# Optimization experiments

Measured on AMD Instinct MI355X. Metric: run time of the kernel, lower is better.

The kernel has to match this reference:

```python
import jax, jax.numpy as jnp
import numpy as np

# Eval-mode reference (dropout disabled), faithful to run_specGCN_lstm(reconstruct_graph=True).

def _run_lstm(x, h0, c0, wih, whh, b):
    # x: [B, T, in]; wih: [4H, in]; torch gate order i, f, g, o
    def step(carry, xt):
        h, c = carry
        g = xt @ wih.T + h @ whh.T + b
        i, f, gg, o = jnp.split(g, 4, axis=-1)
        c = jax.nn.sigmoid(f) * c + jax.nn.sigmoid(i) * jnp.tanh(gg)
        h = jax.nn.sigmoid(o) * jnp.tanh(c)
        return (h, c), h
    (h, c), ys = jax.lax.scan(step, (h0, c0), jnp.swapaxes(x, 0, 1))
    return jnp.swapaxes(ys, 0, 1), h, c


def _lstm2(x, states, wih0, whh0, b0, wih1, whh1, b1):
    (h0, c0), (h1, c1) = states
    y0, hf0, cf0 = _run_lstm(x, h0, c0, wih0, whh0, b0)
    y1, hf1, cf1 = _run_lstm(y0, h1, c1, wih1, whh1, b1)
    return y1, ((hf0, cf0), (hf1, cf1))


def setup_inputs() -> dict:
    key = jax.random.key(0)
    ks = jax.random.split(key, 20)
    B, D, Y, N, F, O, H = 256, 28, 7, 23, 128, 64, 128
    s_gl = 1.0 / np.sqrt(F)
    s_gcn = np.sqrt(6.0 / (F + O)) * 1.414
    s_l0 = 1.0 / np.sqrt(H)
    return {
        "x": jax.random.normal(ks[0], (B, D, N, F), jnp.float32),
        "adj_real": jax.random.uniform(ks[1], (B, D, N, N), jnp.float32),
        "infection": jax.random.uniform(ks[2], (B, D, N), jnp.float32),
        "day_order": jax.random.randint(ks[3], (B,), 0, 10, jnp.int32),
        "gl_w1": jax.random.normal(ks[4], (F, F), jnp.float32) * s_gl,
        "gl_b1": jax.random.normal(ks[5], (F,), jnp.float32) * s_gl,
        "gl_w2": jax.random.normal(ks[6], (F, F), jnp.float32) * s_gl,
        "gl_b2": jax.random.normal(ks[7], (F,), jnp.float32) * s_gl,
        "glp": jax.random.normal(ks[8], (N, N), jnp.float32) * 0.1,
        "gcn_w": jax.random.uniform(ks[9], (F, O), jnp.float32, -s_gcn, s_gcn),
        "v": jnp.full((N,), 0.05, jnp.float32),  # torch init: mean 0.05, std 0
        "lstm_wih0": jax.random.normal(ks[10], (4 * H, O + 1), jnp.float32) * s_l0,
        "lstm_whh0": jax.random.normal(ks[11], (4 * H, H), jnp.float32) * s_l0,
        "lstm_b0": jax.random.normal(ks[12], (4 * H,), jnp.float32) * s_l0,
        "lstm_wih1": jax.random.normal(ks[13], (4 * H, H), jnp.float32) * s_l0,
        "lstm_whh1": jax.random.normal(ks[14], (4 * H, H), jnp.float32) * s_l0,
        "lstm_b1": jax.random.normal(ks[15], (4 * H,), jnp.float32) * s_l0,
        "fc_w": jax.random.normal(ks[16], (1, H + D), jnp.float32) * 0.05,
        "fc_b": jax.random.normal(ks[17], (1,), jnp.float32) * 0.05,
    }


def reference(x, adj_real, infection, day_order, gl_w1, gl_b1, gl_w2, gl_b2,
              glp, gcn_w, v, lstm_wih0, lstm_whh0, lstm_b0, lstm_wih1,
              lstm_whh1, lstm_b1, fc_w, fc_b):
    B, D, N, F = x.shape
    O = gcn_w.shape[1]
    H = lstm_whh0.shape[1]
    Y = 7  # y_days
    alpha = 1.0

    # GraphLearner (alpha = 1)
    n1 = jnp.tanh(alpha * (x @ gl_w1.T + gl_b1))  # [B,D,N,F]
    n2 = jnp.tanh(alpha * (x @ gl_w2.T + gl_b2))
    s12 = jnp.einsum('bdnf,bdmf->bdnm', n1, n2)
    adj_learned = jax.nn.relu(jnp.tanh(alpha * (s12 - jnp.swapaxes(s12, -1, -2))))

    # degree-gated real adjacency
    deg = adj_real.sum(-1)  # [B,D,N]
    mat_deg = jax.nn.sigmoid(glp * (deg[..., :, None] * deg[..., None, :]))
    adj = adj_learned + mat_deg * adj_real  # adj_output [B,D,N,N]

    # SpecGCN: D^-1/2 (A+I) D^-1/2, then X W, relu (dropout off in eval)
    tA = adj + jnp.eye(N, dtype=adj.dtype)
    dinv = tA.sum(-1) ** -0.5
    dad = dinv[..., :, None] * tA * dinv[..., None, :]
    gcn = jax.nn.relu(jnp.einsum('bdnm,bdmo->bdno', dad, x @ gcn_w))  # [B,D,N,O]

    # per-zone temporal decay exp(v^2 * day_order)
    factor = jnp.exp(v * v * day_order.astype(x.dtype)[:, None])  # [B,N]
    gcn = gcn * factor[:, None, :, None]

    lstm_in = jnp.concatenate([gcn, infection[..., None]], axis=-1)  # [B,D,N,O+1]
    zin = jnp.transpose(lstm_in, (2, 0, 1, 3)).reshape(N * B, D, O + 1)

    z0 = jnp.zeros((N * B, H), x.dtype)
    zeros = ((z0, z0), (z0, z0))
    _, states = _lstm2(zin, zeros, lstm_wih0, lstm_whh0, lstm_b0,
                       lstm_wih1, lstm_whh1, lstm_b1)

    x2 = jnp.broadcast_to(zin.mean(axis=1, keepdims=True), (N * B, Y, O + 1))
    out, _ = _lstm2(x2, states, lstm_wih0, lstm_whh0, lstm_b0,
                    lstm_wih1, lstm_whh1, lstm_b1)  # [NB, Y, H]

    inf_feat = jnp.transpose(infection, (2, 0, 1)).reshape(N * B, 1, D)
    inf_feat = jnp.broadcast_to(inf_feat, (N * B, Y, D))
    fc_in = jnp.concatenate([out, inf_feat], axis=-1)  # [NB, Y, H+D]
    y = jax.nn.relu(fc_in @ fc_w.T + fc_b)  # [NB, Y, 1]
    y_out = jnp.transpose(y.reshape(N, B, Y), (1, 2, 0))  # [B, Y, N]
    return adj, y_out
```

## Files before the change

kernel.cpp:

```cpp
#include <hip/hip_runtime.h>
#include <hip/hip_bf16.h>
#include <stdint.h>


#define DB 256
#define DD 28
#define DN 23
#define DF 128
#define DO 64
#define DH 128
#define DY 7
#define NBSEQ (DN*DB)
#define ADJSZ (DB*DD*DN*DN)
#define GBLK 184
#define L2E 1.4426950408889634f

#define WB0_OFF   47480832u
#define WB1_OFF   47710208u
#define WPK_OFF   47972352u
#define GPK_OFF   48103424u

using v8bf  = __attribute__((ext_vector_type(8))) __bf16;
using f32x4 = __attribute__((ext_vector_type(4))) float;
using u32x4 = __attribute__((ext_vector_type(4))) unsigned int;
using u16x4 = __attribute__((ext_vector_type(4))) unsigned short;

__device__ __forceinline__ float fsig(float x)  { return 1.f/(1.f+__expf(-x)); }
__device__ __forceinline__ float ftanh(float x) { return 1.f - 2.f/(__expf(2.f*x)+1.f); }
__device__ __forceinline__ float fsigR(float x){
    return __builtin_amdgcn_rcpf(1.f + __builtin_amdgcn_exp2f(-x*L2E));
}
__device__ __forceinline__ float ftanhR(float x){
    return 1.f - 2.f*__builtin_amdgcn_rcpf(__builtin_amdgcn_exp2f(x*(2.f*L2E))+1.f);
}
__device__ __forceinline__ float fsig2(float a){
    return __builtin_amdgcn_rcpf(1.f + __builtin_amdgcn_exp2f(-a));
}
__device__ __forceinline__ float ftanh2(float a){
    return 1.f - 2.f*__builtin_amdgcn_rcpf(__builtin_amdgcn_exp2f(a)+1.f);
}
__device__ __forceinline__ float ftanhc(float c){
    return 1.f - 2.f*__builtin_amdgcn_rcpf(__builtin_amdgcn_exp2f(c*(2.f*L2E))+1.f);
}

__device__ __forceinline__ unsigned short f2bf(float f){
    unsigned u = __builtin_bit_cast(unsigned, f);
    return (unsigned short)((u + 0x7FFFu + ((u>>16)&1u)) >> 16);
}
__device__ __forceinline__ float bf2f(unsigned short b){
    return __builtin_bit_cast(float, (unsigned)b << 16);
}
__device__ __forceinline__ uint4 ntload4(const uint4* p){
    u32x4 v = __builtin_nontemporal_load((const u32x4*)p);
    return *(uint4*)&v;
}
__device__ __forceinline__ unsigned pkbf(float lo, float hi){
    unsigned r;
    asm("v_cvt_pk_bf16_f32 %0, %1, %2" : "=v"(r) : "v"(lo), "v"(hi));
    return r;
}

#define MFMA_(acc_, A_, B_) acc_ = __builtin_amdgcn_mfma_f32_16x16x32_bf16(A_, B_, acc_, 0, 0, 0)

__global__ __launch_bounds__(256) void kernPrep(
    const float* __restrict__ wih0, const float* __restrict__ whh0,
    const float* __restrict__ wih1, const float* __restrict__ whh1,
    const float* __restrict__ glw1, const float* __restrict__ glw2,
    const float* __restrict__ gcn_w,
    unsigned short* __restrict__ wb0, unsigned short* __restrict__ wb1,
    unsigned short* __restrict__ wpk, unsigned short* __restrict__ gpk)
{
    int idx = blockIdx.x*256 + threadIdx.x;
    if (idx < 114688){
        int e = idx&7, l = (idx>>3)&63, mt = (idx>>9)&31, kt = idx>>14;
        int rit = l&15, lj = rit>>2, g = rit&3;
        int r = g*128 + (mt>>2)*16 + lj*4 + (mt&3);
        int k = kt*32 + (l>>4)*8 + e;
        float v = 0.f;
        if (k < 65)                  v = wih0[r*65 + k];
        else if (k >= 72 && k < 200) v = whh0[r*128 + (k-72)];
        v *= (g==2) ? (2.f*L2E) : L2E;
        wb0[idx] = f2bf(v);
        return;
    }
    idx -= 114688;
    if (idx < 131072){
        int e = idx&7, l = (idx>>3)&63, mt = (idx>>9)&31, kt = idx>>14;
        int rit = l&15, lj = rit>>2, g = rit&3;
        int r = g*128 + (mt>>2)*16 + lj*4 + (mt&3);
        int k = kt*32 + (l>>4)*8 + e;
        float v = (k < 128) ? wih1[r*128 + k] : whh1[r*128 + (k-128)];
        v *= (g==2) ? (2.f*L2E) : L2E;
        wb1[idx] = f2bf(v);
        return;
    }
    idx -= 131072;
    if (idx < 65536){
        int e = idx&7, l = (idx>>3)&63, hsel = (idx>>9)&1, kt = (idx>>10)&3,
            nt = (idx>>12)&7, mat = (idx>>15)&1;
        int fo = nt*16 + (l&15);
        int k  = kt*32 + (l>>4)*8 + e;
        float v = (mat ? glw2 : glw1)[fo*128 + k];
        unsigned short hb = f2bf(v);
        wpk[idx] = hsel ? f2bf(v - bf2f(hb)) : hb;
        return;
    }
    idx -= 65536;
    if (idx < 8192){
        int e = idx&7, l = (idx>>3)&63, kt = (idx>>9)&3, nt = (idx>>11)&3;
        int o = nt*16 + (l&15);
        int k = kt*32 + (l>>4)*8 + e;
        gpk[idx] = f2bf(gcn_w[k*64 + o]);
    }
}

__global__ __launch_bounds__(256) void kernA(
    const float* __restrict__ x, const float* __restrict__ adj_real,
    const float* __restrict__ infection, const int* __restrict__ day_order,
    const float* __restrict__ b1, const float* __restrict__ b2,
    const float* __restrict__ glp, const float* __restrict__ vvec,
    const v8bf* __restrict__ wpk, const v8bf* __restrict__ gpk,
    float* __restrict__ out_adj, uint4* __restrict__ zlin4)
{
    const int bd = blockIdx.x;
    const int b  = bd / DD;
    const int t  = threadIdx.x;
    const int w  = t>>6, l = t&63;

    __shared__ float sm[4140];
    const int S12=0, ADJ=552, XW=1104, DEG=2576, DINV=2599, FACT=2622,
              INFS=2645, GC=2668;
    __shared__ __align__(16) unsigned short xhl[2][32][140];
    __shared__ __align__(16) unsigned short n1b[32*136];
    __shared__ __align__(16) unsigned short n2b[32*136];
    unsigned short* n1l = &xhl[0][0][0];
    unsigned short* n2l = n1l + 32*136;

    {
        const float4* xg4 = (const float4*)(x + (size_t)bd*(DN*DF));
        for (int p=t; p<736; p+=256){
            float4 v = xg4[p];
            int n = p>>5, k4 = (p&31)<<2;
            unsigned short h0=f2bf(v.x), h1=f2bf(v.y), h2=f2bf(v.z), h3=f2bf(v.w);
            u16x4 hv = {h0,h1,h2,h3};
            u16x4 lv = {f2bf(v.x-bf2f(h0)), f2bf(v.y-bf2f(h1)),
                        f2bf(v.z-bf2f(h2)), f2bf(v.w-bf2f(h3))};
            *(u16x4*)&xhl[0][n][k4] = hv;
            *(u16x4*)&xhl[1][n][k4] = lv;
        }
    }
    for (int p=t; p<9*DF; p+=256){
        int n = DN + (p>>7), k = p&127;
        xhl[0][n][k] = 0; xhl[1][n][k] = 0;
    }
    {
        const float* arg = adj_real + (size_t)bd*(DN*DN);
        for (int p=t; p<DN*DN; p+=256){
            int i = p/DN, j = p - i*DN;
            sm[ADJ + i*24 + j] = arg[p];
        }
    }
    {
        uint4 z; z.x=z.y=z.z=z.w=0u;
        for (int i=t; i<306; i+=256){
            int bsel = (i >= 153), off = bsel ? i-153 : i;
            *(uint4*)((char*)(bsel ? n2b : n1b) + 6256 + off*16) = z;
        }
    }
    if (t < DN){
        float vv = vvec[t];
        sm[FACT+t] = __expf(vv*vv*(float)day_order[b]);
        sm[INFS+t] = infection[(size_t)bd*DN + t];
    }
    __syncthreads();

    {
        f32x4 acc2[2];
        { f32x4 z; z[0]=z[1]=z[2]=z[3]=0.f; acc2[0]=z; acc2[1]=z; }
        #pragma unroll
        for (int kt=0;kt<4;kt++){
            v8bf ah[2], al[2];
            #pragma unroll
            for (int mt=0;mt<2;mt++){
                int m = mt*16 + (l&15);
                int ko = (l>>4)*8 + kt*32;
                ah[mt] = *(const v8bf*)&xhl[0][m][ko];
                al[mt] = *(const v8bf*)&xhl[1][m][ko];
            }
            v8bf gh = gpk[(size_t)(w*4+kt)*64 + l];
            MFMA_(acc2[0], ah[0], gh);
            MFMA_(acc2[1], ah[1], gh);
            MFMA_(acc2[0], al[0], gh);
            MFMA_(acc2[1], al[1], gh);
        }
        int o = w*16 + (l&15);
        #pragma unroll
        for (int mt=0;mt<2;mt++){
            #pragma unroll
            for (int r=0;r<4;r++){
                int n = mt*16 + (l>>4)*4 + r;
                if (n < DN) sm[XW + n*64 + o] = acc2[mt][r];
            }
        }
    }

    if (t < DN){
        float s = 0.f;
        for (int m=0;m<DN;m++) s += sm[ADJ + t*24 + m];
        sm[DEG+t] = s;
    }

    {
        const int mat = w>>1;
        const int ntb = (w&1)*4;
        const float* bsrc = mat ? b2 : b1;
        float bias[4];
        #pragma unroll
        for (int q=0;q<4;q++) bias[q] = bsrc[(ntb+q)*16 + (l&15)];
        f32x4 acc[2][4];
        #pragma unroll
        for (int mt=0;mt<2;mt++)
            #pragma unroll
            for (int q=0;q<4;q++){ f32x4 z; z[0]=z[1]=z[2]=z[3]=0.f; acc[mt][q]=z; }
        #pragma unroll
        for (int kt=0;kt<4;kt++){
            v8bf ah[2], al[2];
            #pragma unroll
            for (int mt=0;mt<2;mt++){
                int m = mt*16 + (l&15);
                int ko = (l>>4)*8 + kt*32;
                ah[mt] = *(const v8bf*)&xhl[0][m][ko];
                al[mt] = *(const v8bf*)&xhl[1][m][ko];
            }
            #pragma unroll
            for (int q=0;q<4;q++){
                const v8bf* wb = wpk + ((size_t)(((mat*8+(ntb+q))*4+kt)*2)*64 + l);
                v8bf wh = wb[0], wl = wb[64];
                MFMA_(acc[0][q], ah[0], wh);
                MFMA_(acc[1][q], ah[1], wh);
                MFMA_(acc[0][q], al[0], wh);
                MFMA_(acc[1][q], al[1], wh);
                MFMA_(acc[0][q], ah[0], wl);
                MFMA_(acc[1][q], ah[1], wl);
            }
        }
        __syncthreads();

        unsigned short* dsth = mat ? n2b : n1b;
        unsigned short* dstl = mat ? n2l : n1l;
        #pragma unroll
        for (int mt=0;mt<2;mt++){
            #pragma unroll
            for (int q=0;q<4;q++){
                int fo = (ntb+q)*16 + (l&15);
                #pragma unroll
                for (int r=0;r<4;r++){
                    int n = mt*16 + (l>>4)*4 + r;
                    if (n < DN){
                        float nv = ftanhR(acc[mt][q][r] + bias[q]);
                        unsigned short hb = f2bf(nv);
                        dsth[n*136 + fo] = hb;
                        dstl[n*136 + fo] = f2bf(nv - bf2f(hb));
                    }
                }
            }
        }
        {
            uint4 z; z.x=z.y=z.z=z.w=0u;
            for (int i=t; i<306; i+=256){
                int bsel = (i >= 153), off = bsel ? i-153 : i;
                *(uint4*)((char*)(bsel ? n2l : n1l) + 6256 + off*16) = z;
            }
        }
    }
    __syncthreads();

    {
        const int mt = w>>1, nt = w&1;
        f32x4 a3; a3[0]=a3[1]=a3[2]=a3[3]=0.f;
        #pragma unroll
        for (int kt=0;kt<4;kt++){
            int ar = (mt*16+(l&15))*136 + kt*32 + (l>>4)*8;
            int br = (nt*16+(l&15))*136 + kt*32 + (l>>4)*8;
            v8bf ah  = *(const v8bf*)&n1b[ar];
            v8bf alo = *(const v8bf*)&n1l[ar];
            v8bf bh  = *(const v8bf*)&n2b[br];
            v8bf blo = *(const v8bf*)&n2l[br];
            MFMA_(a3, ah,  bh);
            MFMA_(a3, alo, bh);
            MFMA_(a3, ah,  blo);
        }
        #pragma unroll
        for (int r=0;r<4;r++){
            int i = mt*16 + (l>>4)*4 + r;
            int j = nt*16 + (l&15);
            if (i < DN && j < DN) sm[S12 + i*24 + j] = a3[r];
        }
    }
    __syncthreads();

    for (int p=t; p<DN*DN; p+=256){
        int i=p/DN, j=p-i*DN;
        float al  = fmaxf(ftanhR(sm[S12+i*24+j]-sm[S12+j*24+i]), 0.f);
        float md  = fsigR(glp[i*DN+j]*sm[DEG+i]*sm[DEG+j]);
        float arv = sm[ADJ + i*24 + j];
        float adjv = al + md*arv;
        __builtin_nontemporal_store(adjv, &out_adj[(size_t)bd*(DN*DN) + p]);
        sm[ADJ + i*24 + j] = adjv + (i==j ? 1.f : 0.f);
    }
    __syncthreads();

    if (t<DN){
        float rs=0.f;
        for (int jj=0;jj<DN;jj++) rs += sm[ADJ+t*24+jj];
        sm[DINV+t] = rsqrtf(rs);
    }
    __syncthreads();

    for (int p=t;p<DN*DN;p+=256){
        int i=p/DN, j=p-i*DN;
        sm[ADJ+i*24+j] *= sm[DINV+i]*sm[DINV+j];
    }
    __syncthreads();

    for (int p=t;p<DN*64;p+=256){
        int n=p>>6, o=p&63;
        float a=0.f;
        #pragma unroll
        for (int m=0;m<DN;m++) a = fmaf(sm[ADJ+n*24+m], sm[XW+m*64+o], a);
        sm[GC + p] = fmaxf(a,0.f)*sm[FACT+n];
    }
    __syncthreads();

    for (int p=t; p<DN*18; p+=256){
        int n = p/18, r = p - n*18, hsel = r/9, k8 = r - hsel*9;
        __align__(16) unsigned short ob[8];
        #pragma unroll
        for (int e=0;e<8;e++){
            int k = k8*8+e;
            float v = (k<64) ? sm[GC + n*64 + k] : ((k==64) ? sm[INFS+n] : 0.f);
            unsigned short hb = f2bf(v);
            ob[e] = hsel ? f2bf(v - bf2f(hb)) : hb;
        }
        zlin4[(size_t)bd*414 + p] = *(const uint4*)ob;
    }
}

#define XB0O 0
#define XB1O 4608
#define U1H0 9216
#define U1H1 28672
#define X2O  45056
#define B0O  54272
#define B1O  56320
#define FCO  58368
#define INO  58896
#define C0O  59024
#define C1O  75408

__global__ __launch_bounds__(1024, 2) void kernB(
    const uint4* __restrict__ zlin, const v8bf* __restrict__ w0p, const v8bf* __restrict__ w1p,
    const float* __restrict__ b0g, const float* __restrict__ b1g,
    const float* __restrict__ infection, const float* __restrict__ fcw,
    const float* __restrict__ fcb, float* __restrict__ outy)
{
    const int t = threadIdx.x, blk = blockIdx.x;
    const int w = t>>6, l = t&63;
    const int lhi = l>>4, llo = l&15;
    __shared__ __align__(16) unsigned char smraw[91792];
    char* smb = (char*)smraw;

    {
        uint4 z; z.x=z.y=z.z=z.w=0u;
        for (int i = t; i < (54272-9216)/16; i += 1024) ((uint4*)(smb+9216))[i] = z;
        for (int i = t; i < (91792-59024)/16; i += 1024) ((uint4*)(smb+59024))[i] = z;
    }
    if (t < 512){
        float s = ((t&3)==2) ? (2.f*L2E) : L2E;
        ((float*)(smb+B0O))[t] = b0g[(t&3)*128 + (t>>2)] * s;
        ((float*)(smb+B1O))[t] = b1g[(t&3)*128 + (t>>2)] * s;
    }
    if (t < 129) ((float*)(smb+FCO))[t] = (t<128) ? fcw[t] : fcb[0];
    if (t < 32){
        int gseq = blk*32 + t, n = gseq>>8, bb = gseq&255;
        float a = 0.f;
        for (int dd=0; dd<DD; dd++)
            a = fmaf(fcw[128+dd], infection[((size_t)bb*DD+dd)*DN+n], a);
        ((float*)(smb+INO))[t] = a;
    }

    int k81 = t >> 5, sq1 = t & 31;
    int gs1 = blk*32 + sq1;
    size_t cb1 = (size_t)(gs1 & 255)*DD*414 + (gs1>>8)*18 + k81;
    int d1 = t*16;

    const int mt0 = 2*w;
    const int jt  = mt0>>2, r3 = mt0&3;
    const int j8  = jt*2 + (lhi>>1);
    const int sub = (lhi&1)*8 + r3*2;
    const int j0  = jt*16 + lhi*4 + r3;

    __syncthreads();

    if (t < 288){
        uint4 a0 = ntload4(zlin + cb1);
        *(uint4*)(smb + XB0O + d1) = a0;
    }
    __syncthreads();

    for (int step = 0; step < DD + DY; ++step){
        const int ps  = step & 1;
        const int xb  = ps ? XB1O : XB0O;
        const int xbn = ps ? XB0O : XB1O;
        const bool do_stage = (step + 1 < DD);
        const char* h0rd = smb + U1H0 + (ps^1)*9728;
        char*       h0wr = smb + U1H0 + ps*9728;
        const char* h1rd = smb + U1H1 + (ps^1)*8192;
        char*       h1wr = smb + U1H1 + ps*8192;

        {
            uint4 sv0; sv0.x=sv0.y=sv0.z=sv0.w=0u;
            if (do_stage && t < 288)
                sv0 = ntload4(zlin + (size_t)(step+1)*414 + cb1);

            f32x4 acc[2][2];
            #pragma unroll
            for (int mi=0;mi<2;mi++){
                f32x4 bv = *(const f32x4*)(smb + B0O + (j0+mi)*16);
                acc[mi][0] = bv; acc[mi][1] = bv;
            }
            #pragma unroll 2
            for (int kt=0; kt<7; ++kt){
                const v8bf* wrow = w0p + (size_t)(kt*32 + mt0)*64 + l;
                v8bf A0 = wrow[0], A1 = wrow[64];
                int k8 = kt*4 + lhi;
                bool inx = (k8 <= 8);
                const char* hib = inx ? (smb + xb + k8*512) : (h0rd + (k8-9)*512);
                v8bf BH0 = *(const v8bf*)(hib + llo*16);
                v8bf BH1 = *(const v8bf*)(hib + 256 + llo*16);
                MFMA_(acc[0][0], A0, BH0);
                MFMA_(acc[1][0], A1, BH0);
                MFMA_(acc[0][1], A0, BH1);
                MFMA_(acc[1][1], A1, BH1);
            }
            if (do_stage && t < 288)
                *(uint4*)(smb + xbn + d1) = sv0;

            if (step < DD && t < 288){
                const unsigned short* hp = (const unsigned short*)(smb + xb + t*16);
                float* xs = (float*)(smb + X2O);
                #pragma unroll
                for (int e=0;e<8;e++) xs[e*288+t] += bf2f(hp[e]);
            }

            {
                f32x4 c0v = *(const f32x4*)(smb + C0O + t*16);
                #pragma unroll
                for (int nt=0;nt<2;nt++){
                    float hf[2];
                    #pragma unroll
                    for (int mi=0;mi<2;mi++){
                        f32x4 a = acc[mi][nt];
                        float ii = fsig2(a[0]), ff = fsig2(a[1]), gg = ftanh2(a[2]), oo = fsig2(a[3]);
                        float c = ff*c0v[mi*2+nt] + ii*gg;
                        c0v[mi*2+nt] = c;
                        hf[mi] = oo*ftanhc(c);
                    }
                    unsigned ph = pkbf(hf[0], hf[1]);
                    int bo = j8*512 + (nt*16+llo)*16 + sub;
                    *(unsigned*)(h0wr + bo) = ph;
                }
                *(f32x4*)(smb + C0O + t*16) = c0v;
            }
            __syncthreads();
        }

        {
            f32x4 acc1[2][2];
            #pragma unroll
            for (int mi=0;mi<2;mi++){
                f32x4 bv = *(const f32x4*)(smb + B1O + (j0+mi)*16);
                acc1[mi][0] = bv; acc1[mi][1] = bv;
            }
            #pragma unroll 2
            for (int kt=0; kt<8; ++kt){
                const v8bf* wrow = w1p + (size_t)(kt*32 + mt0)*64 + l;
                v8bf A0 = wrow[0], A1 = wrow[64];
                int k8 = kt*4 + lhi;
                const char* hib = (k8 < 16) ? (h0wr + k8*512) : (h1rd + (k8-16)*512);
                v8bf BH0 = *(const v8bf*)(hib + llo*16);
                v8bf BH1 = *(const v8bf*)(hib + 256 + llo*16);
                MFMA_(acc1[0][0], A0, BH0);
                MFMA_(acc1[1][0], A1, BH0);
                MFMA_(acc1[0][1], A0, BH1);
                MFMA_(acc1[1][1], A1, BH1);
            }

            {
                f32x4 c1v = *(const f32x4*)(smb + C1O + t*16);
                #pragma unroll
                for (int nt=0;nt<2;nt++){
                    float hf[2];
                    #pragma unroll
                    for (int mi=0;mi<2;mi++){
                        f32x4 a = acc1[mi][nt];
                        float ii = fsig2(a[0]), ff = fsig2(a[1]), gg = ftanh2(a[2]), oo = fsig2(a[3]);
                        float c = ff*c1v[mi*2+nt] + ii*gg;
                        c1v[mi*2+nt] = c;
                        hf[mi] = oo*ftanhc(c);
                    }
                    unsigned ph = pkbf(hf[0], hf[1]);
                    int bo = j8*512 + (nt*16+llo)*16 + sub;
                    *(unsigned*)(h1wr + bo) = ph;
                }
                *(f32x4*)(smb + C1O + t*16) = c1v;
            }
        }

        if (step == DD-1){
            __syncthreads();
            if (t < 288){
                const float* xs = (const float*)(smb + X2O);
                __align__(16) unsigned short hb8[8];
                #pragma unroll
                for (int e=0;e<8;e++) hb8[e] = f2bf(xs[e*288+t] * (1.f/(float)DD));
                *(uint4*)(smb + XB0O + t*16) = *(const uint4*)hb8;
                *(uint4*)(smb + XB1O + t*16) = *(const uint4*)hb8;
            }
            __syncthreads();
        }

        if (step >= DD){
            __syncthreads();
            if (t < 256){
                int seq = t>>3, l8 = t&7;
                const unsigned short* uh = (const unsigned short*)(smb + U1H1 + ps*8192);
                const float* fw = (const float*)(smb+FCO);
                float a = 0.f;
                #pragma unroll
                for (int half=0; half<2; ++half){
                    int k8 = l8*2 + half;
                    int base = (k8*32 + seq)*8;
                    #pragma unroll
                    for (int e=0;e<8;e++){
                        int j = l8*16 + half*8 + e;
                        a = fmaf(fw[j], bf2f(uh[base+e]), a);
                    }
                }
                a += __shfl_down(a, 4, 8);
                a += __shfl_down(a, 2, 8);
                a += __shfl_down(a, 1, 8);
                if (l8 == 0){
                    int gseq = blk*32 + seq, n = gseq>>8, bb = gseq&255;
                    float yv = fmaxf(a + ((const float*)(smb+INO))[seq] + fw[128], 0.f);
                    __builtin_nontemporal_store(yv, &outy[((size_t)bb*DY + (step-DD))*DN + n]);
                }
            }
        }
    }
}

extern "C" void kernel_launch(void* const* d_in, const int* in_sizes, int n_in,
                              void* d_out, int out_size, void* d_ws, size_t ws_size,
                              hipStream_t stream)
{
    const float* x         = (const float*)d_in[0];
    const float* adj_real  = (const float*)d_in[1];
    const float* infection = (const float*)d_in[2];
    const int*   day_order = (const int*)  d_in[3];
    const float* gl_w1     = (const float*)d_in[4];
    const float* gl_b1     = (const float*)d_in[5];
    const float* gl_w2     = (const float*)d_in[6];
    const float* gl_b2     = (const float*)d_in[7];
    const float* glp       = (const float*)d_in[8];
    const float* gcn_w     = (const float*)d_in[9];
    const float* vvec      = (const float*)d_in[10];
    const float* wih0      = (const float*)d_in[11];
    const float* whh0      = (const float*)d_in[12];
    const float* b0        = (const float*)d_in[13];
    const float* wih1      = (const float*)d_in[14];
    const float* whh1      = (const float*)d_in[15];
    const float* b1        = (const float*)d_in[16];
    const float* fcw       = (const float*)d_in[17];
    const float* fcb       = (const float*)d_in[18];

    uint8_t* wsb = (uint8_t*)d_ws;
    uint4*          zlin = (uint4*)(wsb);
    unsigned short* wb0  = (unsigned short*)(wsb + WB0_OFF);
    unsigned short* wb1  = (unsigned short*)(wsb + WB1_OFF);
    unsigned short* wpk  = (unsigned short*)(wsb + WPK_OFF);
    unsigned short* gpk  = (unsigned short*)(wsb + GPK_OFF);
    float* out_adj = (float*)d_out;
    float* out_y   = out_adj + ADJSZ;

    kernPrep<<<dim3(1248), dim3(256), 0, stream>>>(wih0, whh0, wih1, whh1,
                                                   gl_w1, gl_w2, gcn_w,
                                                   wb0, wb1, wpk, gpk);
    kernA<<<dim3(DB*DD), dim3(256), 0, stream>>>(x, adj_real, infection, day_order,
                                                 gl_b1, gl_b2, glp, vvec,
                                                 (const v8bf*)wpk, (const v8bf*)gpk,
                                                 out_adj, zlin);
    kernB<<<dim3(GBLK), dim3(1024), 0, stream>>>(zlin, (const v8bf*)wb0,
                                                 (const v8bf*)wb1, b0, b1, infection,
                                                 fcw, fcb, out_y);
}
```

Before: 297.2 us.

## Precompute sequence mean in separate kernel and prefetch first layer-1 weight tile

Moves the time-mean of the LSTM input out of the recurrent kernel into a new small kernel, kernM, that reads zlin and writes a bf16 mean buffer. The recurrent kernel then stages the mean as its input for the prediction steps, which removes the per-step shared-memory accumulation and the two extra barriers at the step boundary. It also loads the first k-tile of the layer-1 weights early so that load overlaps the layer-0 gate math, and it shrinks shared memory. The cost is an extra kernel launch and a re-read of zlin, and the mean is now summed from bf16 hi/lo halves separately, which changes rounding slightly.

```diff
diff --git a/kernel.cpp b/kernel.cpp
--- a/kernel.cpp
+++ b/kernel.cpp
@@ -19,6 +19,7 @@
 #define WB1_OFF   47710208u
 #define WPK_OFF   47972352u
 #define GPK_OFF   48103424u
+#define ZME_OFF   48119808u
 
 using v8bf  = __attribute__((ext_vector_type(8))) __bf16;
 using f32x4 = __attribute__((ext_vector_type(4))) float;
@@ -114,6 +115,30 @@
     }
 }
 
+__global__ __launch_bounds__(256) void kernM(
+    const uint4* __restrict__ zlin, uint4* __restrict__ zmean)
+{
+    int idx = blockIdx.x*256 + threadIdx.x;
+    if (idx >= GBLK*288) return;
+    int blk = idx/288, u = idx - blk*288;
+    int k8 = u>>5, sq = u&31;
+    int gs = blk*32 + sq, bb = gs&255, nn = gs>>8;
+    const uint4* src = zlin + (size_t)bb*DD*414 + nn*18 + k8;
+    float s[8];
+    #pragma unroll
+    for (int e=0;e<8;e++) s[e]=0.f;
+    for (int d=0; d<DD; ++d){
+        uint4 v = src[(size_t)d*414];
+        const unsigned short* hp = (const unsigned short*)&v;
+        #pragma unroll
+        for (int e=0;e<8;e++) s[e] += bf2f(hp[e]);
+    }
+    __align__(16) unsigned short ob[8];
+    #pragma unroll
+    for (int e=0;e<8;e++) ob[e] = f2bf(s[e]*(1.f/(float)DD));
+    zmean[idx] = *(const uint4*)ob;
+}
+
 __global__ __launch_bounds__(256) void kernA(
     const float* __restrict__ x, const float* __restrict__ adj_real,
     const float* __restrict__ infection, const int* __restrict__ day_order,
@@ -350,16 +375,16 @@
 #define XB1O 4608
 #define U1H0 9216
 #define U1H1 28672
-#define X2O  45056
-#define B0O  54272
-#define B1O  56320
-#define FCO  58368
-#define INO  58896
-#define C0O  59024
-#define C1O  75408
+#define B0O  45056
+#define B1O  47104
+#define FCO  49152
+#define INO  49680
+#define C0O  49808
+#define C1O  66192
 
 __global__ __launch_bounds__(1024, 2) void kernB(
-    const uint4* __restrict__ zlin, const v8bf* __restrict__ w0p, const v8bf* __restrict__ w1p,
+    const uint4* __restrict__ zlin, const uint4* __restrict__ zmean,
+    const v8bf* __restrict__ w0p, const v8bf* __restrict__ w1p,
     const float* __restrict__ b0g, const float* __restrict__ b1g,
     const float* __restrict__ infection, const float* __restrict__ fcw,
     const float* __restrict__ fcb, float* __restrict__ outy)
@@ -367,13 +392,13 @@
     const int t = threadIdx.x, blk = blockIdx.x;
     const int w = t>>6, l = t&63;
     const int lhi = l>>4, llo = l&15;
-    __shared__ __align__(16) unsigned char smraw[91792];
+    __shared__ __align__(16) unsigned char smraw[82576];
     char* smb = (char*)smraw;
 
     {
         uint4 z; z.x=z.y=z.z=z.w=0u;
-        for (int i = t; i < (54272-9216)/16; i += 1024) ((uint4*)(smb+9216))[i] = z;
-        for (int i = t; i < (91792-59024)/16; i += 1024) ((uint4*)(smb+59024))[i] = z;
+        for (int i = t; i < (45056-9216)/16; i += 1024) ((uint4*)(smb+9216))[i] = z;
+        for (int i = t; i < (82576-49808)/16; i += 1024) ((uint4*)(smb+49808))[i] = z;
     }
     if (t < 512){
         float s = ((t&3)==2) ? (2.f*L2E) : L2E;
@@ -393,6 +418,7 @@
     int gs1 = blk*32 + sq1;
     size_t cb1 = (size_t)(gs1 & 255)*DD*414 + (gs1>>8)*18 + k81;
     int d1 = t*16;
+    const uint4* zme = zmean + (size_t)blk*288 + t;
 
     const int mt0 = 2*w;
     const int jt  = mt0>>2, r3 = mt0&3;
@@ -412,16 +438,21 @@
         const int ps  = step & 1;
         const int xb  = ps ? XB1O : XB0O;
         const int xbn = ps ? XB0O : XB1O;
-        const bool do_stage = (step + 1 < DD);
+        const bool do_stage = (step + 1 < DD + DY);
         const char* h0rd = smb + U1H0 + (ps^1)*9728;
         char*       h0wr = smb + U1H0 + ps*9728;
         const char* h1rd = smb + U1H1 + (ps^1)*8192;
         char*       h1wr = smb + U1H1 + ps*8192;
 
+        v8bf P0, P1;
+
         {
             uint4 sv0; sv0.x=sv0.y=sv0.z=sv0.w=0u;
-            if (do_stage && t < 288)
-                sv0 = ntload4(zlin + (size_t)(step+1)*414 + cb1);
+            if (do_stage && t < 288){
+                const uint4* src = (step+1 < DD) ? (zlin + (size_t)(step+1)*414 + cb1)
+                                                 : zme;
+                sv0 = ntload4(src);
+            }
 
             f32x4 acc[2][2];
             #pragma unroll
@@ -443,15 +474,14 @@
                 MFMA_(acc[0][1], A0, BH1);
                 MFMA_(acc[1][1], A1, BH1);
             }
+
+            {
+                const v8bf* w1r0 = w1p + (size_t)mt0*64 + l;
+                P0 = w1r0[0]; P1 = w1r0[64];
+            }
+
             if (do_stage && t < 288)
                 *(uint4*)(smb + xbn + d1) = sv0;
-
-            if (step < DD && t < 288){
-                const unsigned short* hp = (const unsigned short*)(smb + xb + t*16);
-                float* xs = (float*)(smb + X2O);
-                #pragma unroll
-                for (int e=0;e<8;e++) xs[e*288+t] += bf2f(hp[e]);
-            }
 
             {
                 f32x4 c0v = *(const f32x4*)(smb + C0O + t*16);
@@ -482,8 +512,17 @@
                 f32x4 bv = *(const f32x4*)(smb + B1O + (j0+mi)*16);
                 acc1[mi][0] = bv; acc1[mi][1] = bv;
             }
+            {
+                const char* hib = h0wr + lhi*512;
+                v8bf BH0 = *(const v8bf*)(hib + llo*16);
+                v8bf BH1 = *(const v8bf*)(hib + 256 + llo*16);
+                MFMA_(acc1[0][0], P0, BH0);
+                MFMA_(acc1[1][0], P1, BH0);
+                MFMA_(acc1[0][1], P0, BH1);
+                MFMA_(acc1[1][1], P1, BH1);
+            }
             #pragma unroll 2
-            for (int kt=0; kt<8; ++kt){
+            for (int kt=1; kt<8; ++kt){
                 const v8bf* wrow = w1p + (size_t)(kt*32 + mt0)*64 + l;
                 v8bf A0 = wrow[0], A1 = wrow[64];
                 int k8 = kt*4 + lhi;
@@ -515,19 +554,6 @@
                 }
                 *(f32x4*)(smb + C1O + t*16) = c1v;
             }
-        }
-
-        if (step == DD-1){
-            __syncthreads();
-            if (t < 288){
-                const float* xs = (const float*)(smb + X2O);
-                __align__(16) unsigned short hb8[8];
-                #pragma unroll
-                for (int e=0;e<8;e++) hb8[e] = f2bf(xs[e*288+t] * (1.f/(float)DD));
-                *(uint4*)(smb + XB0O + t*16) = *(const uint4*)hb8;
-                *(uint4*)(smb + XB1O + t*16) = *(const uint4*)hb8;
-            }
-            __syncthreads();
         }
 
         if (step >= DD){
@@ -585,11 +611,12 @@
     const float* fcb       = (const float*)d_in[18];
 
     uint8_t* wsb = (uint8_t*)d_ws;
-    uint4*          zlin = (uint4*)(wsb);
-    unsigned short* wb0  = (unsigned short*)(wsb + WB0_OFF);
-    unsigned short* wb1  = (unsigned short*)(wsb + WB1_OFF);
-    unsigned short* wpk  = (unsigned short*)(wsb + WPK_OFF);
-    unsigned short* gpk  = (unsigned short*)(wsb + GPK_OFF);
+    uint4*          zlin  = (uint4*)(wsb);
+    unsigned short* wb0   = (unsigned short*)(wsb + WB0_OFF);
+    unsigned short* wb1   = (unsigned short*)(wsb + WB1_OFF);
+    unsigned short* wpk   = (unsigned short*)(wsb + WPK_OFF);
+    unsigned short* gpk   = (unsigned short*)(wsb + GPK_OFF);
+    uint4*          zmean = (uint4*)(wsb + ZME_OFF);
     float* out_adj = (float*)d_out;
     float* out_y   = out_adj + ADJSZ;
 
@@ -600,7 +627,8 @@
                                                  gl_b1, gl_b2, glp, vvec,
                                                  (const v8bf*)wpk, (const v8bf*)gpk,
                                                  out_adj, zlin);
-    kernB<<<dim3(GBLK), dim3(1024), 0, stream>>>(zlin, (const v8bf*)wb0,
+    kernM<<<dim3((GBLK*288+255)/256), dim3(256), 0, stream>>>(zlin, zmean);
+    kernB<<<dim3(GBLK), dim3(1024), 0, stream>>>(zlin, zmean, (const v8bf*)wb0,
                                                  (const v8bf*)wb1, b0, b1, infection,
                                                  fcw, fcb, out_y);
 }
```

Measured after the change: 303.4 us. 2.1% more time.
